# Performance work log

Hardware: AMD Instinct MI355X
Metric: run time of the kernel (lower is better)

The kernel has to match this reference:

```python
import jax, jax.numpy as jnp
import numpy as np

N = 50000
E = 800000
IN_C, HID, LAT = 256, 128, 64


def setup_inputs() -> dict:
    key = jax.random.key(0)
    ks = jax.random.split(key, 8)
    x = jax.random.normal(ks[0], (N, IN_C), dtype=jnp.float32)
    edge_index = jax.random.randint(ks[1], (2, E), 0, N, dtype=jnp.int64)
    # Glorot-ish scaled weights (PyG GCNConv: Linear weight + separate bias)
    W1 = jax.random.normal(ks[2], (IN_C, HID), dtype=jnp.float32) / np.sqrt(IN_C)
    b1 = jnp.zeros((HID,), dtype=jnp.float32)
    Wmu = jax.random.normal(ks[3], (HID, LAT), dtype=jnp.float32) / np.sqrt(HID)
    bmu = jnp.zeros((LAT,), dtype=jnp.float32)
    Wlv = jax.random.normal(ks[4], (HID, LAT), dtype=jnp.float32) / np.sqrt(HID)
    blv = jnp.zeros((LAT,), dtype=jnp.float32)
    return {"x": x, "edge_index": edge_index, "W1": W1, "b1": b1,
            "Wmu": Wmu, "bmu": bmu, "Wlv": Wlv, "blv": blv}


def gcn_conv(x, edge_index, W, b):
    """PyG GCNConv: add self-loops, sym-normalize, transform, scatter-add."""
    n = x.shape[0]
    loop = jnp.arange(n, dtype=edge_index.dtype)
    row = jnp.concatenate([edge_index[0], loop])  # source
    col = jnp.concatenate([edge_index[1], loop])  # target
    deg = jax.ops.segment_sum(jnp.ones_like(col, dtype=x.dtype), col, num_segments=n)
    dinv = jax.lax.rsqrt(jnp.maximum(deg, 1e-12))  # deg >= 1 due to self-loops
    norm = dinv[row] * dinv[col]                   # [E+N]
    h = x @ W                                      # transform first (smaller width)
    msg = h[row] * norm[:, None]                   # [E+N, out] gathered messages
    out = jax.ops.segment_sum(msg, col, num_segments=n)
    return out + b


def reference(x, edge_index, W1, b1, Wmu, bmu, Wlv, blv):
    h = jax.nn.relu(gcn_conv(x, edge_index, W1, b1))
    # dropout p=0.0 -> identity
    mu = gcn_conv(h, edge_index, Wmu, bmu)
    logvar = gcn_conv(h, edge_index, Wlv, blv)
    return (mu, logvar)
```

## Files before the change

kernel.cpp:

```cpp
#include <hip/hip_runtime.h>
#include <stdint.h>

#define NN   50000
#define NE   800000
#define INC  256
#define HID  128
#define LAT  64

typedef unsigned short u16;
typedef short v8s __attribute__((ext_vector_type(8)));
typedef float v4f __attribute__((ext_vector_type(4)));

#define CNT8_OFF 0
#define BKT8_OFF 100000
#define W1P_OFF  3100000
#define W2P_OFF  3116384
#define G1_OFF   3124576

#define G2_OFFU  8388608
#define C2_CNT   8388608
#define C2_DINV  8438608
#define C2_BKT   8488608

#define GB    782

__device__ __forceinline__ u16 f2b(float f) {
    union { float f; uint32_t i; } c; c.f = f;
    uint32_t r = c.i + 0x7FFF + ((c.i >> 16) & 1);
    return (u16)(r >> 16);
}
__device__ __forceinline__ float blo(unsigned u) { return __uint_as_float(u << 16); }
__device__ __forceinline__ float bhi(unsigned u) { return __uint_as_float(u & 0xffff0000u); }

__device__ void pack1_body(const float* __restrict__ W1, u16* __restrict__ W1P, int b) {
    int tg = b * 256 + threadIdx.x;
    int ks = tg >> 9, rem = tg & 511;
    int nt = rem >> 6, lane = rem & 63;
    int quad = lane >> 4, l15 = lane & 15;
    u16 o[8];
    #pragma unroll
    for (int j = 0; j < 8; j++)
        o[j] = f2b(W1[(long)(ks * 32 + quad * 8 + j) * HID + nt * 16 + l15]);
    *(ushort4*)(W1P + (long)tg * 8)     = make_ushort4(o[0], o[1], o[2], o[3]);
    *(ushort4*)(W1P + (long)tg * 8 + 4) = make_ushort4(o[4], o[5], o[6], o[7]);
}

__device__ void pack2_body(const float* __restrict__ Wmu, const float* __restrict__ Wlv,
                           u16* __restrict__ W2P, int b) {
    int tg = b * 256 + threadIdx.x;
    int ks = tg >> 9, rem = tg & 511;
    int nt = rem >> 6, lane = rem & 63;
    int quad = lane >> 4, l15 = lane & 15;
    const float* W = (nt < 4) ? Wmu : Wlv;
    int ntl = (nt < 4) ? nt : nt - 4;
    u16 o[8];
    #pragma unroll
    for (int j = 0; j < 8; j++)
        o[j] = f2b(W[(long)(ks * 32 + quad * 8 + j) * LAT + ntl * 16 + l15]);
    *(ushort4*)(W2P + (long)tg * 8)     = make_ushort4(o[0], o[1], o[2], o[3]);
    *(ushort4*)(W2P + (long)tg * 8 + 4) = make_ushort4(o[4], o[5], o[6], o[7]);
}

__global__ __launch_bounds__(256) void k_fusedA(unsigned* csr, const float* W1,
        const float* Wmu, const float* Wlv) {
    int b = blockIdx.x;
    if (b < 16) pack1_body(W1, (u16*)(csr + W1P_OFF), b);
    else pack2_body(Wmu, Wlv, (u16*)(csr + W2P_OFF), b - 16);
}

__device__ void gemm1_body(const float* __restrict__ xbuf,
        const unsigned* __restrict__ csr, u16* __restrict__ g1, int blk) {
    const u16* W1P = (const u16*)(csr + W1P_OFF);
    int tid = threadIdx.x;
    int lane = tid & 63, w = tid >> 6;
    int quad = lane >> 4, l15 = lane & 15;
    int m0 = blk * 64 + w * 16;
    int arow = m0 + l15;
    int arc = arow < NN ? arow : NN - 1;
    const float* ap = xbuf + (long)arc * INC + quad * 8;
    const v8s* bp = (const v8s*)W1P;
    v4f acc[8];
    #pragma unroll
    for (int t = 0; t < 8; t++) acc[t] = (v4f){0.f, 0.f, 0.f, 0.f};

    #pragma unroll 1
    for (int ks = 0; ks < 8; ks++) {
        float4 a0 = *(const float4*)(ap + ks * 32);
        float4 a1 = *(const float4*)(ap + ks * 32 + 4);
        v8s af;
        af[0] = (short)f2b(a0.x); af[1] = (short)f2b(a0.y);
        af[2] = (short)f2b(a0.z); af[3] = (short)f2b(a0.w);
        af[4] = (short)f2b(a1.x); af[5] = (short)f2b(a1.y);
        af[6] = (short)f2b(a1.z); af[7] = (short)f2b(a1.w);
        #pragma unroll
        for (int t = 0; t < 8; t++) {
            v8s bf = bp[(ks * 8 + t) * 64 + lane];
            acc[t] = __builtin_amdgcn_mfma_f32_16x16x32_bf16(af, bf, acc[t], 0, 0, 0);
        }
    }
    #pragma unroll
    for (int r = 0; r < 4; r++) {
        int rr = m0 + quad * 4 + r;
        if (rr < NN) {
            u16* dst = g1 + (long)rr * HID + l15;
            #pragma unroll
            for (int t = 0; t < 8; t++) dst[t * 16] = f2b(acc[t][r]);
        }
    }
}

__device__ void fill_body(const int* __restrict__ row, const int* __restrict__ col,
                          unsigned* __restrict__ csr, int id, int shard) {
    unsigned* cnt = csr + CNT8_OFF;
    u16* bkt = (u16*)(csr + BKT8_OFF);
    int base = id * 1024 + threadIdx.x;
    unsigned sh8 = 8u * (unsigned)(shard & 3);
    int wsel = shard >> 2;
    #pragma unroll
    for (int i = 0; i < 4; i++) {
        int e = base + 256 * i;
        if (e < NE) {
            int v = col[e];
            unsigned old = atomicAdd(&cnt[v * 2 + wsel], 1u << sh8);
            int slot = (int)((old >> sh8) & 0xffu);
            if (slot < 15) bkt[((shard * NN) + v) * 15 + slot] = (u16)row[e];
        }
    }
}

__global__ __launch_bounds__(256) void k_fusedB(const float* __restrict__ xbuf,
        unsigned* __restrict__ csr, u16* __restrict__ g1,
        const int* __restrict__ row, const int* __restrict__ col) {
    int b = blockIdx.x;
    int g = b >> 3, r = b & 7;
    int id = (g >> 1) * 8 + r;
    if (g & 1) fill_body(row, col, csr, id, r);
    else gemm1_body(xbuf, csr, g1, id);
}

__global__ __launch_bounds__(256) void k_degc(const unsigned* __restrict__ csr,
        unsigned* __restrict__ xb) {
    int tid = threadIdx.x;
    int lane = tid & 63, w = tid >> 6;
    int v = blockIdx.x * 4 + w;
    const unsigned* cnt8 = csr + CNT8_OFF;
    const u16* bkt8 = (const u16*)(csr + BKT8_OFF);
    int* cnt2 = (int*)(xb + C2_CNT);
    float* dinv = (float*)(xb + C2_DINV);
    u16* bkt2 = (u16*)(xb + C2_BKT);
    unsigned w0 = cnt8[v * 2], w1 = cnt8[v * 2 + 1];
    int cl[8];
    int deg = 0, tot = 0;
    #pragma unroll
    for (int x = 0; x < 8; x++) {
        int cx = (int)(((x < 4 ? w0 : w1) >> (8 * (x & 3))) & 0xffu);
        deg += cx;
        cl[x] = cx < 15 ? cx : 15;
        tot += cl[x];
    }
    int cn = tot < 64 ? tot : 64;
    if (lane < cn) {
        int rem = lane, x = 0, more = 1;
        #pragma unroll
        for (int k = 0; k < 7; k++) {
            int take = more && (rem >= cl[k]);
            if (take) { rem -= cl[k]; x = k + 1; }
            more = take;
        }
        bkt2[(v << 6) + lane] = bkt8[((x * NN) + v) * 15 + rem];
    }
    if (lane == 0) { cnt2[v] = cn; dinv[v] = rsqrtf((float)(deg + 1)); }
}

#define ACC8(P, D, W) if (P) { \
    a0 += D * blo(W.x); a1 += D * bhi(W.x); a2 += D * blo(W.y); a3 += D * bhi(W.y); \
    a4 += D * blo(W.z); a5 += D * bhi(W.z); a6 += D * blo(W.w); a7 += D * bhi(W.w); }
#define RED(S) \
    a0 += __shfl_xor(a0, S); a1 += __shfl_xor(a1, S); a2 += __shfl_xor(a2, S); \
    a3 += __shfl_xor(a3, S); a4 += __shfl_xor(a4, S); a5 += __shfl_xor(a5, S); \
    a6 += __shfl_xor(a6, S); a7 += __shfl_xor(a7, S);

__global__ __launch_bounds__(256) void k_gather1(const u16* __restrict__ g1,
        const unsigned* __restrict__ xb, const float* __restrict__ b1,
        u16* __restrict__ h) {
    int tid = threadIdx.x;
    int lane = tid & 63, w = tid >> 6;
    int v = blockIdx.x * 4 + w;
    int q = lane >> 4, c = lane & 15;
    const int* cnt2 = (const int*)(xb + C2_CNT);
    const float* dinv = (const float*)(xb + C2_DINV);
    const u16* bkt2 = (const u16*)(xb + C2_BKT);
    int cn = cnt2[v];
    float dvv = dinv[v];
    int idx = (lane < cn) ? (int)bkt2[(v << 6) + lane] : 0;
    float dvu = dinv[idx];
    float a0 = 0.f, a1 = 0.f, a2 = 0.f, a3 = 0.f, a4 = 0.f, a5 = 0.f, a6 = 0.f, a7 = 0.f;
    if (q == 0) {
        uint4 wv = *(const uint4*)(g1 + (long)v * HID + c * 8);
        a0 = dvv * blo(wv.x); a1 = dvv * bhi(wv.x); a2 = dvv * blo(wv.y); a3 = dvv * bhi(wv.y);
        a4 = dvv * blo(wv.z); a5 = dvv * bhi(wv.z); a6 = dvv * blo(wv.w); a7 = dvv * bhi(wv.w);
    }
    for (int t = 0; t < cn; t += 16) {
        int t0 = t + q, t1 = t0 + 4, t2 = t0 + 8, t3 = t0 + 12;
        bool p0 = t0 < cn, p1 = t1 < cn, p2 = t2 < cn, p3 = t3 < cn;
        int u0 = __shfl(idx, t0), u1 = __shfl(idx, t1),
            u2 = __shfl(idx, t2), u3 = __shfl(idx, t3);
        float d0 = __shfl(dvu, t0), d1 = __shfl(dvu, t1),
              d2 = __shfl(dvu, t2), d3 = __shfl(dvu, t3);
        uint4 w0, w1, w2, w3;
        if (p0) w0 = *(const uint4*)(g1 + (long)u0 * HID + c * 8);
        if (p1) w1 = *(const uint4*)(g1 + (long)u1 * HID + c * 8);
        if (p2) w2 = *(const uint4*)(g1 + (long)u2 * HID + c * 8);
        if (p3) w3 = *(const uint4*)(g1 + (long)u3 * HID + c * 8);
        ACC8(p0, d0, w0)
        ACC8(p1, d1, w1)
        ACC8(p2, d2, w2)
        ACC8(p3, d3, w3)
    }
    RED(16)
    RED(32)
    if (q == 0) {
        int j = c * 8;
        float r[8] = {a0, a1, a2, a3, a4, a5, a6, a7};
        unsigned p[4];
        #pragma unroll
        for (int i = 0; i < 4; i++) {
            float x0 = dvv * r[2 * i]     + b1[j + 2 * i];
            float x1 = dvv * r[2 * i + 1] + b1[j + 2 * i + 1];
            x0 = x0 > 0.f ? x0 : 0.f;
            x1 = x1 > 0.f ? x1 : 0.f;
            p[i] = (unsigned)f2b(x0) | ((unsigned)f2b(x1) << 16);
        }
        uint4 o; o.x = p[0]; o.y = p[1]; o.z = p[2]; o.w = p[3];
        *(uint4*)(h + (long)v * HID + j) = o;
    }
}

__global__ __launch_bounds__(256) void k_gemm2(const u16* __restrict__ h,
        const unsigned* __restrict__ csr, u16* __restrict__ g2) {
    const u16* W2P = (const u16*)(csr + W2P_OFF);
    int tid = threadIdx.x;
    int lane = tid & 63, w = tid >> 6;
    int quad = lane >> 4, l15 = lane & 15;
    int m0 = blockIdx.x * 64 + w * 16;
    int arow = m0 + l15;
    int arc = arow < NN ? arow : NN - 1;
    const u16* ap = h + (long)arc * HID + quad * 8;
    const v8s* bp = (const v8s*)W2P;
    v4f acc[8];
    #pragma unroll
    for (int t = 0; t < 8; t++) acc[t] = (v4f){0.f, 0.f, 0.f, 0.f};

    #pragma unroll 1
    for (int ks = 0; ks < 4; ks++) {
        v8s af = *(const v8s*)(ap + ks * 32);
        #pragma unroll
        for (int t = 0; t < 8; t++) {
            v8s bf = bp[(ks * 8 + t) * 64 + lane];
            acc[t] = __builtin_amdgcn_mfma_f32_16x16x32_bf16(af, bf, acc[t], 0, 0, 0);
        }
    }
    #pragma unroll
    for (int r = 0; r < 4; r++) {
        int rr = m0 + quad * 4 + r;
        if (rr < NN) {
            u16* dst = g2 + (long)rr * HID + l15;
            #pragma unroll
            for (int t = 0; t < 8; t++) dst[t * 16] = f2b(acc[t][r]);
        }
    }
}

__global__ __launch_bounds__(256) void k_gather2(const u16* __restrict__ g2,
        const unsigned* __restrict__ xb, const float* __restrict__ bmu,
        const float* __restrict__ blv, float* __restrict__ out) {
    int tid = threadIdx.x;
    int lane = tid & 63, w = tid >> 6;
    int v = blockIdx.x * 4 + w;
    int q = lane >> 4, c = lane & 15;
    const int* cnt2 = (const int*)(xb + C2_CNT);
    const float* dinv = (const float*)(xb + C2_DINV);
    const u16* bkt2 = (const u16*)(xb + C2_BKT);
    int cn = cnt2[v];
    float dvv = dinv[v];
    int idx = (lane < cn) ? (int)bkt2[(v << 6) + lane] : 0;
    float dvu = dinv[idx];
    float a0 = 0.f, a1 = 0.f, a2 = 0.f, a3 = 0.f, a4 = 0.f, a5 = 0.f, a6 = 0.f, a7 = 0.f;
    if (q == 0) {
        uint4 wv = *(const uint4*)(g2 + (long)v * HID + c * 8);
        a0 = dvv * blo(wv.x); a1 = dvv * bhi(wv.x); a2 = dvv * blo(wv.y); a3 = dvv * bhi(wv.y);
        a4 = dvv * blo(wv.z); a5 = dvv * bhi(wv.z); a6 = dvv * blo(wv.w); a7 = dvv * bhi(wv.w);
    }
    for (int t = 0; t < cn; t += 16) {
        int t0 = t + q, t1 = t0 + 4, t2 = t0 + 8, t3 = t0 + 12;
        bool p0 = t0 < cn, p1 = t1 < cn, p2 = t2 < cn, p3 = t3 < cn;
        int u0 = __shfl(idx, t0), u1 = __shfl(idx, t1),
            u2 = __shfl(idx, t2), u3 = __shfl(idx, t3);
        float d0 = __shfl(dvu, t0), d1 = __shfl(dvu, t1),
              d2 = __shfl(dvu, t2), d3 = __shfl(dvu, t3);
        uint4 w0, w1, w2, w3;
        if (p0) w0 = *(const uint4*)(g2 + (long)u0 * HID + c * 8);
        if (p1) w1 = *(const uint4*)(g2 + (long)u1 * HID + c * 8);
        if (p2) w2 = *(const uint4*)(g2 + (long)u2 * HID + c * 8);
        if (p3) w3 = *(const uint4*)(g2 + (long)u3 * HID + c * 8);
        ACC8(p0, d0, w0)
        ACC8(p1, d1, w1)
        ACC8(p2, d2, w2)
        ACC8(p3, d3, w3)
    }
    RED(16)
    RED(32)
    if (q == 0) {
        float r[8] = {a0, a1, a2, a3, a4, a5, a6, a7};
        if (c < 8) {
            int j = c * 8;
            float4 o0 = make_float4(dvv * r[0] + bmu[j],     dvv * r[1] + bmu[j + 1],
                                    dvv * r[2] + bmu[j + 2], dvv * r[3] + bmu[j + 3]);
            float4 o1 = make_float4(dvv * r[4] + bmu[j + 4], dvv * r[5] + bmu[j + 5],
                                    dvv * r[6] + bmu[j + 6], dvv * r[7] + bmu[j + 7]);
            float* dst = out + (long)v * LAT + j;
            *(float4*)dst = o0;
            *(float4*)(dst + 4) = o1;
        } else {
            int j = c * 8 - 64;
            float4 o0 = make_float4(dvv * r[0] + blv[j],     dvv * r[1] + blv[j + 1],
                                    dvv * r[2] + blv[j + 2], dvv * r[3] + blv[j + 3]);
            float4 o1 = make_float4(dvv * r[4] + blv[j + 4], dvv * r[5] + blv[j + 5],
                                    dvv * r[6] + blv[j + 6], dvv * r[7] + blv[j + 7]);
            float* dst = out + (long)NN * LAT + (long)v * LAT + j;
            *(float4*)dst = o0;
            *(float4*)(dst + 4) = o1;
        }
    }
}

extern "C" void kernel_launch(void* const* d_in, const int* in_sizes, int n_in,
                              void* d_out, int out_size, void* d_ws, size_t ws_size,
                              hipStream_t stream) {
    float* xbuf = (float*)d_in[0];
    const int* ei  = (const int*)d_in[1];
    const float* W1  = (const float*)d_in[2];
    const float* b1  = (const float*)d_in[3];
    const float* Wmu = (const float*)d_in[4];
    const float* bmu = (const float*)d_in[5];
    const float* Wlv = (const float*)d_in[6];
    const float* blv = (const float*)d_in[7];
    const int* row = ei;
    const int* col = ei + NE;

    unsigned* csr = (unsigned*)d_out;
    u16* g1   = (u16*)(csr + G1_OFF);
    u16* hbuf = (u16*)xbuf;
    u16* g2   = (u16*)xbuf + G2_OFFU;
    unsigned* xb = (unsigned*)xbuf;

    hipMemsetAsync(csr + CNT8_OFF, 0, 100000 * sizeof(unsigned), stream);
    k_fusedA<<<24, 256, 0, stream>>>(csr, W1, Wmu, Wlv);

    k_fusedB<<<1568, 256, 0, stream>>>(xbuf, csr, g1, row, col);
    k_degc  <<<NN / 4, 256, 0, stream>>>(csr, xb);
    k_gather1<<<NN / 4, 256, 0, stream>>>(g1, xb, b1, hbuf);

    k_gemm2 <<<GB, 256, 0, stream>>>(hbuf, csr, g2);
    k_gather2<<<NN / 4, 256, 0, stream>>>(g2, xb, bmu, blv, (float*)d_out);
}
```

Measured before the change: 232.4 us.

## Replace atomic bucket fill with two-phase LDS partition and per-bin merge

Edge-to-CSR construction moves from global atomics on packed 8-bit per-shard counters to a two-phase scheme. Each block first partitions 1024 edges by destination bin (256 nodes) in shared memory and writes sorted slabs plus offsets. Then one block per bin merges all slabs into per-node buckets using LDS atomics. This removes the memset and the global atomic contention, and it also drops the 15-per-shard truncation. The cost is a merge kernel with only 196 blocks, each serially scanning 784 slabs, which may leave the GPU underused.

```diff
diff --git a/kernel.cpp b/kernel.cpp
--- a/kernel.cpp
+++ b/kernel.cpp
@@ -11,11 +11,15 @@
 typedef short v8s __attribute__((ext_vector_type(8)));
 typedef float v4f __attribute__((ext_vector_type(4)));
 
-#define CNT8_OFF 0
-#define BKT8_OFF 100000
-#define W1P_OFF  3100000
-#define W2P_OFF  3116384
-#define G1_OFF   3124576
+#define SLAB_OFF 0
+#define OFFS_OFF 802816
+#define W1P_OFF  881216
+#define W2P_OFF  897600
+#define G1_OFF   905792
+
+#define NBIN        196
+#define OFFS_STRIDE 200
+#define NSLAB       784
 
 #define G2_OFFU  8388608
 #define C2_CNT   8388608
@@ -109,23 +113,50 @@
     }
 }
 
-__device__ void fill_body(const int* __restrict__ row, const int* __restrict__ col,
-                          unsigned* __restrict__ csr, int id, int shard) {
-    unsigned* cnt = csr + CNT8_OFF;
-    u16* bkt = (u16*)(csr + BKT8_OFF);
-    int base = id * 1024 + threadIdx.x;
-    unsigned sh8 = 8u * (unsigned)(shard & 3);
-    int wsel = shard >> 2;
+__device__ void part_body(const int* __restrict__ row, const int* __restrict__ col,
+                          unsigned* __restrict__ csr, int id) {
+    __shared__ int hist[256];
+    __shared__ int scanbuf[256];
+    __shared__ unsigned recs[1024];
+    int tid = threadIdx.x;
+    int base = id * 1024;
+    hist[tid] = 0;
+    __syncthreads();
+    int v[4], u[4];
     #pragma unroll
     for (int i = 0; i < 4; i++) {
-        int e = base + 256 * i;
+        int e = base + i * 256 + tid;
         if (e < NE) {
-            int v = col[e];
-            unsigned old = atomicAdd(&cnt[v * 2 + wsel], 1u << sh8);
-            int slot = (int)((old >> sh8) & 0xffu);
-            if (slot < 15) bkt[((shard * NN) + v) * 15 + slot] = (u16)row[e];
-        }
-    }
+            v[i] = col[e]; u[i] = row[e];
+            atomicAdd(&hist[v[i] >> 8], 1);
+        } else v[i] = -1;
+    }
+    __syncthreads();
+    int x = hist[tid];
+    scanbuf[tid] = x;
+    __syncthreads();
+    for (int s = 1; s < 256; s <<= 1) {
+        int y = (tid >= s) ? scanbuf[tid - s] : 0;
+        __syncthreads();
+        scanbuf[tid] += y;
+        __syncthreads();
+    }
+    int excl = scanbuf[tid] - x;
+    u16* offs = (u16*)(csr + OFFS_OFF) + (long)id * OFFS_STRIDE;
+    if (tid <= NBIN) offs[tid] = (u16)excl;
+    hist[tid] = excl;
+    __syncthreads();
+    #pragma unroll
+    for (int i = 0; i < 4; i++) {
+        if (v[i] >= 0) {
+            int slot = atomicAdd(&hist[v[i] >> 8], 1);
+            recs[slot] = (unsigned)u[i] | ((unsigned)(v[i] & 255) << 16);
+        }
+    }
+    __syncthreads();
+    unsigned* slab = csr + SLAB_OFF + (long)id * 1024;
+    #pragma unroll
+    for (int i = 0; i < 4; i++) slab[i * 256 + tid] = recs[i * 256 + tid];
 }
 
 __global__ __launch_bounds__(256) void k_fusedB(const float* __restrict__ xbuf,
@@ -134,42 +165,52 @@
     int b = blockIdx.x;
     int g = b >> 3, r = b & 7;
     int id = (g >> 1) * 8 + r;
-    if (g & 1) fill_body(row, col, csr, id, r);
+    if (g & 1) part_body(row, col, csr, id);
     else gemm1_body(xbuf, csr, g1, id);
 }
 
-__global__ __launch_bounds__(256) void k_degc(const unsigned* __restrict__ csr,
+__global__ __launch_bounds__(256) void k_merge(const unsigned* __restrict__ csr,
         unsigned* __restrict__ xb) {
-    int tid = threadIdx.x;
-    int lane = tid & 63, w = tid >> 6;
-    int v = blockIdx.x * 4 + w;
-    const unsigned* cnt8 = csr + CNT8_OFF;
-    const u16* bkt8 = (const u16*)(csr + BKT8_OFF);
+    __shared__ int cnt_lds[256];
+    __shared__ u16 bkt_lds[256 * 64];
+    int tid = threadIdx.x;
+    int bin = blockIdx.x;
+    cnt_lds[tid] = 0;
+    __syncthreads();
+    const u16* offs = (const u16*)(csr + OFFS_OFF);
+    const unsigned* slab = csr + SLAB_OFF;
+    for (int s = tid; s < NSLAB; s += 256) {
+        int st = offs[s * OFFS_STRIDE + bin];
+        int en = offs[s * OFFS_STRIDE + bin + 1];
+        for (int j = st; j < en; j++) {
+            unsigned r = slab[s * 1024 + j];
+            int vlo = (int)(r >> 16);
+            int slot = atomicAdd(&cnt_lds[vlo], 1);
+            if (slot < 64) bkt_lds[(vlo << 6) + slot] = (u16)(r & 0xffffu);
+        }
+    }
+    __syncthreads();
     int* cnt2 = (int*)(xb + C2_CNT);
     float* dinv = (float*)(xb + C2_DINV);
     u16* bkt2 = (u16*)(xb + C2_BKT);
-    unsigned w0 = cnt8[v * 2], w1 = cnt8[v * 2 + 1];
-    int cl[8];
-    int deg = 0, tot = 0;
-    #pragma unroll
-    for (int x = 0; x < 8; x++) {
-        int cx = (int)(((x < 4 ? w0 : w1) >> (8 * (x & 3))) & 0xffu);
-        deg += cx;
-        cl[x] = cx < 15 ? cx : 15;
-        tot += cl[x];
-    }
-    int cn = tot < 64 ? tot : 64;
-    if (lane < cn) {
-        int rem = lane, x = 0, more = 1;
-        #pragma unroll
-        for (int k = 0; k < 7; k++) {
-            int take = more && (rem >= cl[k]);
-            if (take) { rem -= cl[k]; x = k + 1; }
-            more = take;
-        }
-        bkt2[(v << 6) + lane] = bkt8[((x * NN) + v) * 15 + rem];
-    }
-    if (lane == 0) { cnt2[v] = cn; dinv[v] = rsqrtf((float)(deg + 1)); }
+    int v0 = bin << 8;
+    {
+        int v = v0 + tid;
+        if (v < NN) {
+            int deg = cnt_lds[tid];
+            int cn = deg < 64 ? deg : 64;
+            cnt2[v] = cn;
+            dinv[v] = rsqrtf((float)(deg + 1));
+        }
+    }
+    const uint4* src = (const uint4*)bkt_lds;
+    #pragma unroll
+    for (int i = 0; i < 8; i++) {
+        int idx = i * 256 + tid;
+        int node = idx >> 3;
+        if (v0 + node < NN)
+            ((uint4*)(bkt2 + ((long)(v0 + node) << 6)))[idx & 7] = src[idx];
+    }
 }
 
 #define ACC8(P, D, W) if (P) { \
@@ -354,11 +395,10 @@
     u16* g2   = (u16*)xbuf + G2_OFFU;
     unsigned* xb = (unsigned*)xbuf;
 
-    hipMemsetAsync(csr + CNT8_OFF, 0, 100000 * sizeof(unsigned), stream);
     k_fusedA<<<24, 256, 0, stream>>>(csr, W1, Wmu, Wlv);
 
     k_fusedB<<<1568, 256, 0, stream>>>(xbuf, csr, g1, row, col);
-    k_degc  <<<NN / 4, 256, 0, stream>>>(csr, xb);
+    k_merge <<<NBIN, 256, 0, stream>>>(csr, xb);
     k_gather1<<<NN / 4, 256, 0, stream>>>(g1, xb, b1, hbuf);
 
     k_gemm2 <<<GB, 256, 0, stream>>>(hbuf, csr, g2);
```

Result: faster. 223.7 us (-3.7%).
